# Kernel tuning notes

Measured on AMD Instinct MI355X. Metric: run time of the kernel, lower is better.

## Reference

```python
import jax, jax.numpy as jnp
import numpy as np

N, E, F_IN = 100000, 600000, 128
HID, NCLS = 128, 2
# ratio=0.8 applied three times: ceil(0.8*100000), ceil(0.8*80000), ceil(0.8*64000)
K1, K2, K3 = 80000, 64000, 51200


def setup_inputs() -> dict:
    key = jax.random.key(0)
    k = jax.random.split(key, 16)
    s = 0.05
    p = {}
    p['x'] = jax.random.normal(k[0], (N, F_IN), dtype=jnp.float32)
    p['edge_index'] = jax.random.randint(k[1], (2, E), 0, N)
    # GraphConv i: out = lin_rel(sum_j x_j) + lin_root(x_i); lin_root has no bias (PyG)
    p['Wr1'] = jax.random.normal(k[2], (HID, F_IN), jnp.float32) * s
    p['br1'] = jnp.zeros((HID,), jnp.float32)
    p['Wroot1'] = jax.random.normal(k[3], (HID, F_IN), jnp.float32) * s
    p['pw1'] = jax.random.normal(k[4], (HID,), jnp.float32) * s
    p['Wr2'] = jax.random.normal(k[5], (HID, HID), jnp.float32) * s
    p['br2'] = jnp.zeros((HID,), jnp.float32)
    p['Wroot2'] = jax.random.normal(k[6], (HID, HID), jnp.float32) * s
    p['pw2'] = jax.random.normal(k[7], (HID,), jnp.float32) * s
    p['Wr3'] = jax.random.normal(k[8], (HID, HID), jnp.float32) * s
    p['br3'] = jnp.zeros((HID,), jnp.float32)
    p['Wroot3'] = jax.random.normal(k[9], (HID, HID), jnp.float32) * s
    p['pw3'] = jax.random.normal(k[10], (HID,), jnp.float32) * s
    p['W_lin1'] = jax.random.normal(k[11], (HID, 2 * HID), jnp.float32) * s
    p['b_lin1'] = jnp.zeros((HID,), jnp.float32)
    p['W_lin2'] = jax.random.normal(k[12], (64, HID), jnp.float32) * s
    p['b_lin2'] = jnp.zeros((64,), jnp.float32)
    p['W_lin3'] = jax.random.normal(k[13], (NCLS, 64), jnp.float32) * s
    p['b_lin3'] = jnp.zeros((NCLS,), jnp.float32)
    return p


def _gconv(x, src, dst, emask, Wr, br, Wroot):
    # PyG GraphConv(aggr='add'): masked edges contribute zero (== removed edge)
    msg = x[src] * emask[:, None].astype(x.dtype)           # [E, F]
    agg = jax.ops.segment_sum(msg, dst, num_segments=x.shape[0])
    return agg @ Wr.T + br + x @ Wroot.T


def _topk_pool(x, src, dst, emask, w, k):
    # PyG TopKPooling: score = tanh((x.w)/||w||); keep top-k nodes; x = x[perm]*score[perm]
    score = jnp.tanh((x @ w) / jnp.linalg.norm(w))
    vals, perm = jax.lax.top_k(score, k)
    x_new = x[perm] * vals[:, None]
    new_idx = jnp.full((x.shape[0],), -1, jnp.int32).at[perm].set(
        jnp.arange(k, dtype=jnp.int32))
    ns, nd = new_idx[src], new_idx[dst]
    valid = emask & (ns >= 0) & (nd >= 0)
    return x_new, jnp.where(valid, ns, 0), jnp.where(valid, nd, 0), valid


def _readout(x):
    # single graph (batch=None): gmp || gap -> [1, 2F]
    return jnp.concatenate([x.max(axis=0), x.mean(axis=0)])[None, :]


def reference(x, edge_index, Wr1, br1, Wroot1, pw1, Wr2, br2, Wroot2, pw2,
              Wr3, br3, Wroot3, pw3, W_lin1, b_lin1, W_lin2, b_lin2, W_lin3, b_lin3):
    src = edge_index[0].astype(jnp.int32)
    dst = edge_index[1].astype(jnp.int32)
    emask = jnp.ones((src.shape[0],), dtype=bool)

    h = jax.nn.relu(_gconv(x, src, dst, emask, Wr1, br1, Wroot1))
    h, src, dst, emask = _topk_pool(h, src, dst, emask, pw1, K1)
    r1 = _readout(h)

    h = jax.nn.relu(_gconv(h, src, dst, emask, Wr2, br2, Wroot2))
    h, src, dst, emask = _topk_pool(h, src, dst, emask, pw2, K2)
    r2 = _readout(h)

    h = jax.nn.relu(_gconv(h, src, dst, emask, Wr3, br3, Wroot3))
    h, src, dst, emask = _topk_pool(h, src, dst, emask, pw3, K3)
    r3 = _readout(h)

    z = r1 + r2 + r3                                        # [1, 256]
    z = jax.nn.relu(z @ W_lin1.T + b_lin1)                  # dropout: inference no-op
    z = jax.nn.relu(z @ W_lin2.T + b_lin2)
    return z @ W_lin3.T + b_lin3                            # [1, num_classes]
```

## Files before the change

kernel.cpp:

```cpp
#include <hip/hip_runtime.h>
#include <hip/hip_bf16.h>
#include <math.h>

#define N0 100000
#define E0 600000
#define KP1 80000
#define KP2 64000
#define KP3 51200
#define F 128
#define SCAN_CHUNK 1024
#define NCHUNK ((N0 + SCAN_CHUNK - 1) / SCAN_CHUNK)
#define MAXGB 6400

typedef __attribute__((ext_vector_type(8))) short short8;
typedef __attribute__((ext_vector_type(8))) unsigned short ushort8;
typedef __attribute__((ext_vector_type(4))) float f32x4;

__device__ __forceinline__ unsigned fkey(float f) {
    unsigned u = __float_as_uint(f);
    return u ^ ((u & 0x80000000u) ? 0xFFFFFFFFu : 0x80000000u);
}
__device__ __forceinline__ unsigned short f2b(float f) {
    __hip_bfloat16 h = __float2bfloat16(f);
    return *(unsigned short*)&h;
}
__device__ __forceinline__ float b2f(unsigned short u) {
    __hip_bfloat16 h;
    *(unsigned short*)&h = u;
    return __bfloat162float(h);
}

__global__ __launch_bounds__(256) void cvt4K(const float* __restrict__ in,
                                             unsigned short* __restrict__ out, int n4,
                                             unsigned* __restrict__ bar, unsigned* __restrict__ hist,
                                             unsigned* __restrict__ cnt, int* __restrict__ orig) {
    int i = blockIdx.x * 256 + threadIdx.x;
    if (blockIdx.x == 0) {
        if (threadIdx.x < 16) bar[threadIdx.x] = 0u;
        hist[threadIdx.x] = 0u;
    }
    if (i < N0) { cnt[i] = 0u; orig[i] = i; }
    if (i >= n4) return;
    float4 v = *(const float4*)(in + (size_t)i * 4);
    *(ushort4*)(out + (size_t)i * 4) = make_ushort4(f2b(v.x), f2b(v.y), f2b(v.z), f2b(v.w));
}

__global__ __launch_bounds__(256) void cvtWAllK(const float* __restrict__ a0, const float* __restrict__ a1,
                                                const float* __restrict__ a2, const float* __restrict__ a3,
                                                const float* __restrict__ a4, const float* __restrict__ a5,
                                                unsigned short* __restrict__ o) {
    int m = blockIdx.y;
    const float* src = (m == 0) ? a0 : (m == 1) ? a1 : (m == 2) ? a2 : (m == 3) ? a3 : (m == 4) ? a4 : a5;
    int i = blockIdx.x * 256 + threadIdx.x;
    float4 v = *(const float4*)(src + (size_t)i * 4);
    *(ushort4*)(o + (size_t)m * 16384 + (size_t)i * 4) = make_ushort4(f2b(v.x), f2b(v.y), f2b(v.z), f2b(v.w));
}

__global__ __launch_bounds__(128) void pwnK(const float* __restrict__ p0, const float* __restrict__ p1,
                                            const float* __restrict__ p2, float* __restrict__ pwn) {
    __shared__ float sh[128];
    int l = blockIdx.x, t = threadIdx.x;
    const float* p = (l == 0) ? p0 : (l == 1) ? p1 : p2;
    float v = p[t];
    sh[t] = v * v;
    __syncthreads();
    for (int off = 64; off; off >>= 1) {
        if (t < off) sh[t] += sh[t + off];
        __syncthreads();
    }
    pwn[l * 128 + t] = v / sqrtf(sh[0]);
}

__global__ __launch_bounds__(256) void histDstK(const int* __restrict__ dst, unsigned* __restrict__ cnt) {
    int e = blockIdx.x * 256 + threadIdx.x;
    if (e < E0) atomicAdd(&cnt[dst[e]], 1u);
}

__global__ __launch_bounds__(256) void scanReduceK(const unsigned* __restrict__ cnt,
                                                   unsigned* __restrict__ chunkSum, int nbins) {
    __shared__ unsigned sh[256];
    int base = blockIdx.x * SCAN_CHUNK + threadIdx.x * 4;
    unsigned s = 0;
#pragma unroll
    for (int i = 0; i < 4; i++) { int b = base + i; if (b < nbins) s += cnt[b]; }
    sh[threadIdx.x] = s;
    __syncthreads();
    for (int off = 128; off; off >>= 1) {
        if (threadIdx.x < off) sh[threadIdx.x] += sh[threadIdx.x + off];
        __syncthreads();
    }
    if (threadIdx.x == 0) chunkSum[blockIdx.x] = sh[0];
}

__global__ void scanChunksK(const unsigned* __restrict__ chunkSum, unsigned* __restrict__ chunkOff,
                            int nchunks, unsigned* __restrict__ totalOut) {
    if (threadIdx.x == 0) {
        unsigned run = 0;
        for (int i = 0; i < nchunks; i++) { chunkOff[i] = run; run += chunkSum[i]; }
        *totalOut = run;
    }
}

__global__ __launch_bounds__(256) void scanFinalK(const unsigned* __restrict__ cntIn,
                                                  unsigned* __restrict__ cnt,
                                                  const unsigned* __restrict__ chunkOff,
                                                  unsigned* __restrict__ rowptr, int nbins) {
    __shared__ unsigned sh[256];
    int t = threadIdx.x;
    int base = blockIdx.x * SCAN_CHUNK + t * 4;
    unsigned c[4], s = 0;
#pragma unroll
    for (int i = 0; i < 4; i++) { int b = base + i; c[i] = (b < nbins) ? cntIn[b] : 0u; s += c[i]; }
    sh[t] = s;
    __syncthreads();
    for (int off = 1; off < 256; off <<= 1) {
        unsigned v = (t >= off) ? sh[t - off] : 0u;
        __syncthreads();
        sh[t] += v;
        __syncthreads();
    }
    unsigned basep = chunkOff[blockIdx.x] + sh[t] - s;
#pragma unroll
    for (int i = 0; i < 4; i++) {
        int b = base + i;
        if (b < nbins) { rowptr[b] = basep; basep += c[i]; cnt[b] = 0u; }
    }
}

__global__ __launch_bounds__(256) void scatterFillK(const int* __restrict__ src,
                                                    const int* __restrict__ dst,
                                                    const unsigned* __restrict__ rowptr,
                                                    unsigned* __restrict__ fill,
                                                    int* __restrict__ sortedSrc) {
    int e = blockIdx.x * 256 + threadIdx.x;
    if (e >= E0) return;
    int d = dst[e];
    unsigned p = rowptr[d] + atomicAdd(&fill[d], 1u);
    sortedSrc[p] = src[e];
}

__global__ __launch_bounds__(256) void aggSegB(const unsigned short* __restrict__ x,
                                               const int* __restrict__ srcCur,
                                               const unsigned* __restrict__ rowptr,
                                               const int* __restrict__ orig,
                                               unsigned short* __restrict__ agg, int n) {
    int g = blockIdx.x * 16 + (threadIdx.x >> 4);
    int q = threadIdx.x & 15;
    if (g >= n) return;
    int d = orig[g];
    unsigned e0 = rowptr[d], e1 = rowptr[d + 1];
    float a[8];
#pragma unroll
    for (int j = 0; j < 8; j++) a[j] = 0.f;
    unsigned e = e0;
    for (; e + 4 <= e1; e += 4) {
        int s0 = srcCur[e], s1 = srcCur[e + 1], s2 = srcCur[e + 2], s3 = srcCur[e + 3];
        ushort8 v0 = *(const ushort8*)(x + (size_t)(s0 < 0 ? 0 : s0) * F + q * 8);
        ushort8 v1 = *(const ushort8*)(x + (size_t)(s1 < 0 ? 0 : s1) * F + q * 8);
        ushort8 v2 = *(const ushort8*)(x + (size_t)(s2 < 0 ? 0 : s2) * F + q * 8);
        ushort8 v3 = *(const ushort8*)(x + (size_t)(s3 < 0 ? 0 : s3) * F + q * 8);
        float m0 = s0 < 0 ? 0.f : 1.f, m1 = s1 < 0 ? 0.f : 1.f;
        float m2 = s2 < 0 ? 0.f : 1.f, m3 = s3 < 0 ? 0.f : 1.f;
#pragma unroll
        for (int j = 0; j < 8; j++) {
            a[j] = fmaf(b2f(v0[j]), m0, a[j]);
            a[j] = fmaf(b2f(v1[j]), m1, a[j]);
            a[j] = fmaf(b2f(v2[j]), m2, a[j]);
            a[j] = fmaf(b2f(v3[j]), m3, a[j]);
        }
    }
    for (; e < e1; e++) {
        int s = srcCur[e];
        if (s < 0) continue;
        ushort8 v = *(const ushort8*)(x + (size_t)s * F + q * 8);
#pragma unroll
        for (int j = 0; j < 8; j++) a[j] += b2f(v[j]);
    }
    ushort8 o;
#pragma unroll
    for (int j = 0; j < 8; j++) o[j] = f2b(a[j]);
    *(ushort8*)(agg + (size_t)g * F + q * 8) = o;
}

#define CPAD 40
__global__ __launch_bounds__(256) void convM(const unsigned short* __restrict__ A0,
                                             const unsigned short* __restrict__ A1,
                                             const unsigned short* __restrict__ W0,
                                             const unsigned short* __restrict__ W1,
                                             const float* __restrict__ br,
                                             const float* __restrict__ pwn,
                                             unsigned short* __restrict__ hbf,
                                             float* __restrict__ sc,
                                             unsigned* __restrict__ keys,
                                             unsigned* __restrict__ hist,
                                             unsigned* __restrict__ st,
                                             unsigned* __restrict__ done,
                                             int n, int k, int nbGrid) {
    __shared__ unsigned short As[128 * CPAD];
    __shared__ unsigned short Bs[128 * CPAD];
    __shared__ unsigned selh[256];
    int tid = threadIdx.x;
    int w = tid >> 6, l = tid & 63;
    int r = l & 15, g = l >> 4;
    int bm = blockIdx.x * 128;
    int srow = tid >> 2, q4 = tid & 3;

    selh[tid] = 0u;

    f32x4 acc[2][8];
#pragma unroll
    for (int m = 0; m < 2; m++)
#pragma unroll
        for (int c = 0; c < 8; c++) acc[m][c] = (f32x4){0.f, 0.f, 0.f, 0.f};

    for (int ph = 0; ph < 2; ph++) {
        const unsigned short* A = ph ? A1 : A0;
        const unsigned short* W = ph ? W1 : W0;
        for (int kk = 0; kk < 128; kk += 32) {
            __syncthreads();
#pragma unroll
            for (int h2 = 0; h2 < 2; h2++) {
                int rr = srow + h2 * 64;
                uint4 av = make_uint4(0u, 0u, 0u, 0u);
                if (bm + rr < n) av = *(const uint4*)(A + (size_t)(bm + rr) * F + kk + q4 * 8);
                *(uint4*)(&As[rr * CPAD + q4 * 8]) = av;
                uint4 wv = *(const uint4*)(W + (size_t)rr * F + kk + q4 * 8);
                *(uint4*)(&Bs[rr * CPAD + q4 * 8]) = wv;
            }
            __syncthreads();
            short8 af[2], bf[8];
#pragma unroll
            for (int m = 0; m < 2; m++)
                af[m] = *(const short8*)(&As[(w * 32 + m * 16 + r) * CPAD + g * 8]);
#pragma unroll
            for (int c = 0; c < 8; c++)
                bf[c] = *(const short8*)(&Bs[(c * 16 + r) * CPAD + g * 8]);
#pragma unroll
            for (int m = 0; m < 2; m++)
#pragma unroll
                for (int c = 0; c < 8; c++)
                    acc[m][c] = __builtin_amdgcn_mfma_f32_16x16x32_bf16(af[m], bf[c], acc[m][c], 0, 0, 0);
        }
    }

    float pd[2][4];
#pragma unroll
    for (int m = 0; m < 2; m++)
#pragma unroll
        for (int j = 0; j < 4; j++) pd[m][j] = 0.f;

#pragma unroll
    for (int c = 0; c < 8; c++) {
        int col = c * 16 + r;
        float bias = br[col];
        float pwc = pwn[col];
#pragma unroll
        for (int m = 0; m < 2; m++) {
#pragma unroll
            for (int j = 0; j < 4; j++) {
                int row = bm + w * 32 + m * 16 + g * 4 + j;
                float h = fmaxf(acc[m][c][j] + bias, 0.f);
                pd[m][j] += h * pwc;
                if (row < n) hbf[(size_t)row * F + col] = f2b(h);
            }
        }
    }
#pragma unroll
    for (int m = 0; m < 2; m++) {
#pragma unroll
        for (int j = 0; j < 4; j++) {
            float p = pd[m][j];
            p += __shfl_xor(p, 1);
            p += __shfl_xor(p, 2);
            p += __shfl_xor(p, 4);
            p += __shfl_xor(p, 8);
            if (r == 0) {
                int row = bm + w * 32 + m * 16 + g * 4 + j;
                if (row < n) {
                    float s = tanhf(p);
                    sc[row] = s;
                    unsigned key = fkey(s);
                    keys[row] = key;
                    atomicAdd(&selh[key >> 24], 1u);
                }
            }
        }
    }

    __syncthreads();
    if (selh[tid]) atomicAdd(&hist[tid], selh[tid]);
    __syncthreads();
    __shared__ bool lastS;
    if (tid == 0) {
        __threadfence();
        lastS = (atomicAdd(done, 1u) == (unsigned)(nbGrid - 1));
    }
    __syncthreads();
    if (!lastS) return;
    selh[tid] = atomicExch(&hist[tid], 0u);
    __syncthreads();
    if (tid == 0) {
        unsigned krem = (unsigned)k, cum = 0, pfx = 0;
        for (int bch = 255; bch >= 0; bch--) {
            unsigned cc = selh[bch];
            if (cum + cc >= krem) {
                pfx = ((unsigned)bch) << 24;
                krem -= cum;
                break;
            }
            cum += cc;
        }
        atomicExch(&st[0], pfx);
        atomicExch(&st[1], krem);
        *done = 0u;
    }
}

__global__ __launch_bounds__(256) void histSelK(const unsigned* __restrict__ keys, int n,
                                                int p, unsigned* __restrict__ st,
                                                unsigned* __restrict__ hist,
                                                unsigned* __restrict__ done, int nb) {
    __shared__ unsigned lh[256];
    __shared__ bool last;
    int tid = threadIdx.x;
    lh[tid] = 0;
    __syncthreads();
    unsigned prefix = st[0];
    int i = blockIdx.x * 256 + tid;
    if (i < n) {
        unsigned key = keys[i];
        bool m = ((key >> (32 - 8 * p)) == (prefix >> (32 - 8 * p)));
        if (m) atomicAdd(&lh[(key >> (24 - 8 * p)) & 255u], 1u);
    }
    __syncthreads();
    if (lh[tid]) atomicAdd(&hist[tid], lh[tid]);
    __syncthreads();
    if (tid == 0) {
        __threadfence();
        last = (atomicAdd(done, 1u) == (unsigned)(nb - 1));
    }
    __syncthreads();
    if (!last) return;
    lh[tid] = atomicExch(&hist[tid], 0u);
    __syncthreads();
    if (tid == 0) {
        unsigned krem = st[1], cum = 0;
        for (int b = 255; b >= 0; b--) {
            unsigned c = lh[b];
            if (cum + c >= krem) {
                st[0] |= ((unsigned)b) << (24 - 8 * p);
                st[1] = krem - cum;
                break;
            }
            cum += c;
        }
        *done = 0u;
    }
}

__global__ __launch_bounds__(256) void countsK(const unsigned* __restrict__ keys, int n,
                                               const unsigned* __restrict__ st,
                                               unsigned* __restrict__ bGT, unsigned* __restrict__ bEQ,
                                               unsigned* __restrict__ sGT, unsigned* __restrict__ sEQ,
                                               unsigned* __restrict__ done, int nb) {
    __shared__ int cg_, ce_;
    __shared__ bool last;
    int tid = threadIdx.x;
    if (tid == 0) { cg_ = 0; ce_ = 0; }
    __syncthreads();
    unsigned t = st[0];
    int g = 0, e = 0;
    for (int it = 0; it < 4; it++) {
        int i = blockIdx.x * 1024 + it * 256 + tid;
        if (i < n) {
            unsigned k = keys[i];
            g += (k > t);
            e += (k == t);
        }
    }
    atomicAdd(&cg_, g);
    atomicAdd(&ce_, e);
    __syncthreads();
    if (tid == 0) {
        bGT[blockIdx.x] = (unsigned)cg_;
        bEQ[blockIdx.x] = (unsigned)ce_;
        __threadfence();
        last = (atomicAdd(done, 1u) == (unsigned)(nb - 1));
    }
    __syncthreads();
    if (!last) return;
    if (tid == 0) {
        unsigned gs = 0, es = 0;
        for (int b = 0; b < nb; b++) {
            atomicExch(&sGT[b], gs);
            atomicExch(&sEQ[b], es);
            gs += atomicAdd(&bGT[b], 0u);
            es += atomicAdd(&bEQ[b], 0u);
        }
        *done = 0u;
    }
}

__global__ __launch_bounds__(256) void markOrigK(const unsigned* __restrict__ keys, int n,
                                                 const unsigned* __restrict__ st,
                                                 const unsigned* __restrict__ sGT,
                                                 const unsigned* __restrict__ sEQ,
                                                 int* __restrict__ nidx,
                                                 const int* __restrict__ origIn,
                                                 int* __restrict__ origOut, int doNext) {
    __shared__ int wG[4], wE[4];
    __shared__ int runG, runE;
    int tid = threadIdx.x, wv = tid >> 6, lane = tid & 63;
    if (tid == 0) { runG = 0; runE = 0; }
    unsigned t = st[0];
    int needEq = (int)st[1];
    int gOff = (int)atomicAdd((unsigned*)&sGT[blockIdx.x], 0u);
    int eOff = (int)atomicAdd((unsigned*)&sEQ[blockIdx.x], 0u);
    unsigned long long mlt = (((unsigned long long)1) << lane) - 1ull;
    __syncthreads();
    for (int it = 0; it < 4; it++) {
        int i = blockIdx.x * 1024 + it * 256 + tid;
        bool inb = i < n;
        unsigned k = inb ? keys[i] : 0u;
        bool pG = inb && (k > t), pE = inb && (k == t);
        unsigned long long bG = __ballot(pG), bE = __ballot(pE);
        int lpG = __popcll(bG & mlt), lpE = __popcll(bE & mlt);
        if (lane == 0) { wG[wv] = __popcll(bG); wE[wv] = __popcll(bE); }
        __syncthreads();
        int woG = 0, woE = 0;
        for (int w = 0; w < wv; w++) { woG += wG[w]; woE += wE[w]; }
        int gB = gOff + runG + woG + lpG;
        int eB = eOff + runE + woE + lpE;
        int ni = -1;
        if (pG) ni = gB + (eB < needEq ? eB : needEq);
        else if (pE && eB < needEq) ni = gB + eB;
        if (inb) {
            nidx[i] = ni;
            if (doNext && ni >= 0) origOut[ni] = origIn[i];
        }
        __syncthreads();
        if (tid == 0) {
            runG += wG[0] + wG[1] + wG[2] + wG[3];
            runE += wE[0] + wE[1] + wE[2] + wE[3];
        }
        __syncthreads();
    }
}

__global__ __launch_bounds__(256) void gatherRK(const unsigned short* __restrict__ hbf,
                                                const float* __restrict__ sc,
                                                const int* __restrict__ nidx,
                                                const int* __restrict__ srcIn,
                                                int* __restrict__ srcOut,
                                                unsigned short* __restrict__ bufB,
                                                float* __restrict__ pmax, float* __restrict__ psum,
                                                int n, int doNext) {
    __shared__ float redm[256 * 8];
    __shared__ float reds[256 * 8];
    int tid = threadIdx.x, b = blockIdx.x;
    int q = tid & 15;
    int i = b * 16 + (tid >> 4);
    float lm[8], ls[8];
#pragma unroll
    for (int j = 0; j < 8; j++) { lm[j] = -INFINITY; ls[j] = 0.f; }
    if (i < n) {
        int ni = nidx[i];
        if (ni >= 0) {
            float s = sc[i];
            ushort8 v = *(const ushort8*)(hbf + (size_t)i * F + q * 8);
            ushort8 o;
#pragma unroll
            for (int j = 0; j < 8; j++) {
                float prod = b2f(v[j]) * s;
                o[j] = f2b(prod);
                lm[j] = fmaxf(lm[j], prod);
                ls[j] += prod;
            }
            *(ushort8*)(bufB + (size_t)ni * F + q * 8) = o;
        }
    }
    if (doNext) {
        int nbg = gridDim.x;
        for (int e = b * 256 + tid; e < E0; e += nbg * 256) {
            int s2 = srcIn[e];
            srcOut[e] = (s2 >= 0) ? nidx[s2] : -1;
        }
    }
#pragma unroll
    for (int j = 0; j < 8; j++) { redm[tid * 8 + j] = lm[j]; reds[tid * 8 + j] = ls[j]; }
    __syncthreads();
    if (tid < 16) {
        for (int g2 = 1; g2 < 16; g2++) {
#pragma unroll
            for (int j = 0; j < 8; j++) {
                lm[j] = fmaxf(lm[j], redm[(g2 * 16 + tid) * 8 + j]);
                ls[j] += reds[(g2 * 16 + tid) * 8 + j];
            }
        }
#pragma unroll
        for (int j = 0; j < 8; j++) {
            pmax[(size_t)b * 128 + tid * 8 + j] = lm[j];
            psum[(size_t)b * 128 + tid * 8 + j] = ls[j];
        }
    }
}

__global__ __launch_bounds__(128) void rfinal2K(const float* __restrict__ pmax,
                                                const float* __restrict__ psum,
                                                unsigned* __restrict__ pm2, unsigned* __restrict__ ps2,
                                                float* __restrict__ r, unsigned* __restrict__ done,
                                                int np, int k, int initR) {
    int t = threadIdx.x, b = blockIdx.x;
    float m = -INFINITY, s = 0.f;
    for (int row = b; row < np; row += 64) {
        m = fmaxf(m, pmax[(size_t)row * 128 + t]);
        s += psum[(size_t)row * 128 + t];
    }
    atomicExch(&pm2[b * 128 + t], __float_as_uint(m));
    atomicExch(&ps2[b * 128 + t], __float_as_uint(s));
    __syncthreads();
    __shared__ bool last;
    if (t == 0) {
        __threadfence();
        last = (atomicAdd(done, 1u) == 63u);
    }
    __syncthreads();
    if (!last) return;
    m = -INFINITY; s = 0.f;
    for (int bb = 0; bb < 64; bb++) {
        m = fmaxf(m, __uint_as_float(atomicAdd(&pm2[bb * 128 + t], 0u)));
        s += __uint_as_float(atomicAdd(&ps2[bb * 128 + t], 0u));
    }
    if (initR) { r[t] = m; r[128 + t] = s / (float)k; }
    else       { r[t] += m; r[128 + t] += s / (float)k; }
    if (t == 0) *done = 0u;
}

__global__ __launch_bounds__(256) void mlpK(const float* __restrict__ r,
                                            const float* __restrict__ W1, const float* __restrict__ b1,
                                            const float* __restrict__ W2, const float* __restrict__ b2,
                                            const float* __restrict__ W3, const float* __restrict__ b3,
                                            float* __restrict__ out) {
    __shared__ float z0[256], z1[128], z2[64];
    int t = threadIdx.x;
    z0[t] = r[t];
    __syncthreads();
    if (t < 128) {
        float a = b1[t];
        for (int kk = 0; kk < 256; kk++) a = fmaf(W1[t * 256 + kk], z0[kk], a);
        z1[t] = fmaxf(a, 0.f);
    }
    __syncthreads();
    if (t < 64) {
        float a = b2[t];
        for (int kk = 0; kk < 128; kk++) a = fmaf(W2[t * 128 + kk], z1[kk], a);
        z2[t] = fmaxf(a, 0.f);
    }
    __syncthreads();
    if (t < 2) {
        float a = b3[t];
        for (int kk = 0; kk < 64; kk++) a = fmaf(W3[t * 64 + kk], z2[kk], a);
        out[t] = a;
    }
}

extern "C" void kernel_launch(void* const* d_in, const int* in_sizes, int n_in,
                              void* d_out, int out_size, void* d_ws, size_t ws_size,
                              hipStream_t stream) {
    const float* x = (const float*)d_in[0];
    const int* ei = (const int*)d_in[1];
    const float* Wr[3]    = { (const float*)d_in[2],  (const float*)d_in[6],  (const float*)d_in[10] };
    const float* br[3]    = { (const float*)d_in[3],  (const float*)d_in[7],  (const float*)d_in[11] };
    const float* Wroot[3] = { (const float*)d_in[4],  (const float*)d_in[8],  (const float*)d_in[12] };
    const float* pw[3]    = { (const float*)d_in[5],  (const float*)d_in[9],  (const float*)d_in[13] };
    const float* W1 = (const float*)d_in[14];
    const float* b1 = (const float*)d_in[15];
    const float* W2 = (const float*)d_in[16];
    const float* b2 = (const float*)d_in[17];
    const float* W3 = (const float*)d_in[18];
    const float* b3 = (const float*)d_in[19];
    float* out = (float*)d_out;
    char* w = (char*)d_ws;

    size_t o = 0;
    auto alc = [&](size_t bytes) { size_t r = o; o += (bytes + 255) & ~(size_t)255; return r; };
    unsigned short* hbf    = (unsigned short*)(w + alc((size_t)N0 * F * 2));
    unsigned short* xbf    = (unsigned short*)(w + alc((size_t)N0 * F * 2));
    unsigned short* aggbf  = (unsigned short*)(w + alc((size_t)N0 * F * 2));
    unsigned short* bufBbf = (unsigned short*)(w + alc((size_t)KP1 * F * 2));
    unsigned short* wbf    = (unsigned short*)(w + alc((size_t)6 * 16384 * 2));
    float*    pwn    = (float*)(w + alc(3 * 128 * 4));
    float*    sc     = (float*)(w + alc((size_t)N0 * 4));
    unsigned* keys   = (unsigned*)(w + alc((size_t)N0 * 4));
    int*      nidx   = (int*)(w + alc((size_t)N0 * 4));
    int*      sSrc0  = (int*)(w + alc((size_t)E0 * 4));
    int*      srcCA  = (int*)(w + alc((size_t)E0 * 4));
    int*      srcCB  = (int*)(w + alc((size_t)E0 * 4));
    unsigned* cnt    = (unsigned*)(w + alc((size_t)N0 * 4));
    unsigned* rowptr = (unsigned*)(w + alc((size_t)(N0 + 1) * 4));
    int*      origA  = (int*)(w + alc((size_t)N0 * 4));
    int*      origB  = (int*)(w + alc((size_t)N0 * 4));
    unsigned* chS    = (unsigned*)(w + alc(NCHUNK * 4));
    unsigned* chO    = (unsigned*)(w + alc(NCHUNK * 4));
    unsigned* hist   = (unsigned*)(w + alc(256 * 4));
    unsigned* st     = (unsigned*)(w + alc(64));
    unsigned* barA   = (unsigned*)(w + alc(16 * 4));
    unsigned* bGT    = (unsigned*)(w + alc(128 * 4));
    unsigned* bEQ    = (unsigned*)(w + alc(128 * 4));
    unsigned* sGT    = (unsigned*)(w + alc(128 * 4));
    unsigned* sEQ    = (unsigned*)(w + alc(128 * 4));
    float*    r      = (float*)(w + alc(256 * 4));
    float*    pmax   = (float*)(w + alc((size_t)MAXGB * F * 4));
    float*    psum   = (float*)(w + alc((size_t)MAXGB * F * 4));
    unsigned* pm2    = (unsigned*)(w + alc(64 * 128 * 4));
    unsigned* ps2    = (unsigned*)(w + alc(64 * 128 * 4));
    if (o > ws_size) return;

    const int* srcOrig = ei;
    const int* dstOrig = ei + E0;

    cvt4K<<<(N0 * F / 4 + 255) / 256, 256, 0, stream>>>(x, xbf, N0 * F / 4, barA, hist, cnt, origA);
    cvtWAllK<<<dim3(16, 6), 256, 0, stream>>>(Wr[0], Wroot[0], Wr[1], Wroot[1], Wr[2], Wroot[2], wbf);
    pwnK<<<3, 128, 0, stream>>>(pw[0], pw[1], pw[2], pwn);
    histDstK<<<(E0 + 255) / 256, 256, 0, stream>>>(dstOrig, cnt);
    scanReduceK<<<NCHUNK, 256, 0, stream>>>(cnt, chS, N0);
    scanChunksK<<<1, 1, 0, stream>>>(chS, chO, NCHUNK, rowptr + N0);
    scanFinalK<<<NCHUNK, 256, 0, stream>>>(cnt, cnt, chO, rowptr, N0);
    scatterFillK<<<(E0 + 255) / 256, 256, 0, stream>>>(srcOrig, dstOrig, rowptr, cnt, sSrc0);

    unsigned* doneA = barA + 8;

    const int ns[3] = { N0, KP1, KP2 };
    const int ks[3] = { KP1, KP2, KP3 };
    const int* srcCur[3] = { sSrc0, srcCA, srcCB };
    int* srcNext[3] = { srcCA, srcCB, srcCA };
    const int* origCur[3] = { origA, origB, origA };
    int* origNext[3] = { origB, origA, origB };

    for (int L = 0; L < 3; L++) {
        int n = ns[L], k = ks[L];
        const unsigned short* xinbf = (L == 0) ? xbf : bufBbf;
        int doNext = (L < 2) ? 1 : 0;

        aggSegB<<<(n + 15) / 16, 256, 0, stream>>>(xinbf, srcCur[L], rowptr, origCur[L], aggbf, n);
        int nbc = (n + 127) / 128;
        convM<<<nbc, 256, 0, stream>>>(aggbf, xinbf,
                                       wbf + (size_t)(L * 2) * 16384,
                                       wbf + (size_t)(L * 2 + 1) * 16384,
                                       br[L], pwn + L * 128, hbf, sc, keys,
                                       hist, st, doneA, n, k, nbc);
        int nbh = (n + 255) / 256;
        for (int p = 1; p < 4; p++)
            histSelK<<<nbh, 256, 0, stream>>>(keys, n, p, st, hist, doneA, nbh);
        int nb = (n + 1023) / 1024;
        countsK<<<nb, 256, 0, stream>>>(keys, n, st, bGT, bEQ, sGT, sEQ, doneA, nb);
        markOrigK<<<nb, 256, 0, stream>>>(keys, n, st, sGT, sEQ, nidx, origCur[L], origNext[L], doNext);
        int nbg = (n + 15) / 16;
        gatherRK<<<nbg, 256, 0, stream>>>(hbf, sc, nidx, srcCur[L], srcNext[L], bufBbf, pmax, psum, n, doNext);
        rfinal2K<<<64, 128, 0, stream>>>(pmax, psum, pm2, ps2, r, doneA, nbg, k, (L == 0) ? 1 : 0);
    }

    mlpK<<<1, 256, 0, stream>>>(r, W1, b1, W2, b2, W3, b3, out);
}
```

Measured before the change: 718.0 us.

## Preload full weight tile in LDS and coalesce convM output stores via LDS

```diff
diff --git a/kernel.cpp b/kernel.cpp
--- a/kernel.cpp
+++ b/kernel.cpp
@@ -183,6 +183,7 @@
 }
 
 #define CPAD 40
+#define BSTR 136
 __global__ __launch_bounds__(256) void convM(const unsigned short* __restrict__ A0,
                                              const unsigned short* __restrict__ A1,
                                              const unsigned short* __restrict__ W0,
@@ -196,8 +197,10 @@
                                              unsigned* __restrict__ st,
                                              unsigned* __restrict__ done,
                                              int n, int k, int nbGrid) {
-    __shared__ unsigned short As[128 * CPAD];
-    __shared__ unsigned short Bs[128 * CPAD];
+    __shared__ union {
+        struct { unsigned short As[128 * CPAD]; unsigned short Bs[128 * BSTR]; } s;
+        unsigned short Cs[128 * BSTR];
+    } u;
     __shared__ unsigned selh[256];
     int tid = threadIdx.x;
     int w = tid >> 6, l = tid & 63;
@@ -216,25 +219,32 @@
     for (int ph = 0; ph < 2; ph++) {
         const unsigned short* A = ph ? A1 : A0;
         const unsigned short* W = ph ? W1 : W0;
+        __syncthreads();
+        {
+            int col = tid >> 1, hf = tid & 1;
+#pragma unroll
+            for (int i2 = 0; i2 < 8; i2++) {
+                uint4 wv = *(const uint4*)(W + (size_t)col * F + hf * 64 + i2 * 8);
+                *(uint4*)(&u.s.Bs[col * BSTR + hf * 64 + i2 * 8]) = wv;
+            }
+        }
         for (int kk = 0; kk < 128; kk += 32) {
-            __syncthreads();
+            if (kk) __syncthreads();
 #pragma unroll
             for (int h2 = 0; h2 < 2; h2++) {
                 int rr = srow + h2 * 64;
                 uint4 av = make_uint4(0u, 0u, 0u, 0u);
                 if (bm + rr < n) av = *(const uint4*)(A + (size_t)(bm + rr) * F + kk + q4 * 8);
-                *(uint4*)(&As[rr * CPAD + q4 * 8]) = av;
-                uint4 wv = *(const uint4*)(W + (size_t)rr * F + kk + q4 * 8);
-                *(uint4*)(&Bs[rr * CPAD + q4 * 8]) = wv;
+                *(uint4*)(&u.s.As[rr * CPAD + q4 * 8]) = av;
             }
             __syncthreads();
             short8 af[2], bf[8];
 #pragma unroll
             for (int m = 0; m < 2; m++)
-                af[m] = *(const short8*)(&As[(w * 32 + m * 16 + r) * CPAD + g * 8]);
+                af[m] = *(const short8*)(&u.s.As[(w * 32 + m * 16 + r) * CPAD + g * 8]);
 #pragma unroll
             for (int c = 0; c < 8; c++)
-                bf[c] = *(const short8*)(&Bs[(c * 16 + r) * CPAD + g * 8]);
+                bf[c] = *(const short8*)(&u.s.Bs[(c * 16 + r) * BSTR + kk + g * 8]);
 #pragma unroll
             for (int m = 0; m < 2; m++)
 #pragma unroll
@@ -249,6 +259,7 @@
 #pragma unroll
         for (int j = 0; j < 4; j++) pd[m][j] = 0.f;
 
+    __syncthreads();
 #pragma unroll
     for (int c = 0; c < 8; c++) {
         int col = c * 16 + r;
@@ -258,10 +269,22 @@
         for (int m = 0; m < 2; m++) {
 #pragma unroll
             for (int j = 0; j < 4; j++) {
-                int row = bm + w * 32 + m * 16 + g * 4 + j;
+                int rl = w * 32 + m * 16 + g * 4 + j;
                 float h = fmaxf(acc[m][c][j] + bias, 0.f);
                 pd[m][j] += h * pwc;
-                if (row < n) hbf[(size_t)row * F + col] = f2b(h);
+                u.Cs[rl * BSTR + col] = f2b(h);
+            }
+        }
+    }
+    __syncthreads();
+    {
+        int rl = tid >> 1, hf = tid & 1;
+        int grow = bm + rl;
+        if (grow < n) {
+#pragma unroll
+            for (int i2 = 0; i2 < 8; i2++) {
+                uint4 v = *(const uint4*)(&u.Cs[rl * BSTR + hf * 64 + i2 * 8]);
+                *(uint4*)(&hbf[(size_t)grow * F + hf * 64 + i2 * 8]) = v;
             }
         }
     }
@@ -365,6 +388,7 @@
                                                unsigned* __restrict__ done, int nb) {
     __shared__ int cg_, ce_;
     __shared__ bool last;
+    __shared__ unsigned sgl[128], seq[128];
     int tid = threadIdx.x;
     if (tid == 0) { cg_ = 0; ce_ = 0; }
     __syncthreads();
@@ -389,13 +413,15 @@
     }
     __syncthreads();
     if (!last) return;
+    if (tid < nb && tid < 128) { sgl[tid] = atomicAdd(&bGT[tid], 0u); seq[tid] = atomicAdd(&bEQ[tid], 0u); }
+    __syncthreads();
     if (tid == 0) {
         unsigned gs = 0, es = 0;
         for (int b = 0; b < nb; b++) {
             atomicExch(&sGT[b], gs);
             atomicExch(&sEQ[b], es);
-            gs += atomicAdd(&bGT[b], 0u);
-            es += atomicAdd(&bEQ[b], 0u);
+            gs += sgl[b];
+            es += seq[b];
         }
         *done = 0u;
     }
@@ -527,6 +553,7 @@
     __syncthreads();
     if (!last) return;
     m = -INFINITY; s = 0.f;
+#pragma unroll 8
     for (int bb = 0; bb < 64; bb++) {
         m = fmaxf(m, __uint_as_float(atomicAdd(&pm2[bb * 128 + t], 0u)));
         s += __uint_as_float(atomicAdd(&ps2[bb * 128 + t], 0u));
```

Result: faster. 642.0 us (-10.6%).

## Shrink conv GEMM tile to 64 rows, prefetch K-slices, swap MFMA operands

Applied to the files above, without the earlier changes.

```diff
diff --git a/kernel.cpp b/kernel.cpp
--- a/kernel.cpp
+++ b/kernel.cpp
@@ -196,95 +196,76 @@
                                              unsigned* __restrict__ st,
                                              unsigned* __restrict__ done,
                                              int n, int k, int nbGrid) {
-    __shared__ unsigned short As[128 * CPAD];
+    __shared__ unsigned short As[64 * CPAD];
     __shared__ unsigned short Bs[128 * CPAD];
     __shared__ unsigned selh[256];
     int tid = threadIdx.x;
     int w = tid >> 6, l = tid & 63;
     int r = l & 15, g = l >> 4;
-    int bm = blockIdx.x * 128;
+    int bm = blockIdx.x * 64;
     int srow = tid >> 2, q4 = tid & 3;
 
     selh[tid] = 0u;
 
-    f32x4 acc[2][8];
-#pragma unroll
-    for (int m = 0; m < 2; m++)
-#pragma unroll
-        for (int c = 0; c < 8; c++) acc[m][c] = (f32x4){0.f, 0.f, 0.f, 0.f};
-
+    f32x4 acc[8];
+#pragma unroll
+    for (int c = 0; c < 8; c++) acc[c] = (f32x4){0.f, 0.f, 0.f, 0.f};
+
+    int rowA = bm + srow;
     for (int ph = 0; ph < 2; ph++) {
         const unsigned short* A = ph ? A1 : A0;
         const unsigned short* W = ph ? W1 : W0;
-        for (int kk = 0; kk < 128; kk += 32) {
+        uint4 av = make_uint4(0u, 0u, 0u, 0u);
+        if (rowA < n) av = *(const uint4*)(A + (size_t)rowA * F + q4 * 8);
+        uint4 wv0 = *(const uint4*)(W + (size_t)srow * F + q4 * 8);
+        uint4 wv1 = *(const uint4*)(W + (size_t)(srow + 64) * F + q4 * 8);
+        for (int kki = 0; kki < 4; kki++) {
             __syncthreads();
-#pragma unroll
-            for (int h2 = 0; h2 < 2; h2++) {
-                int rr = srow + h2 * 64;
-                uint4 av = make_uint4(0u, 0u, 0u, 0u);
-                if (bm + rr < n) av = *(const uint4*)(A + (size_t)(bm + rr) * F + kk + q4 * 8);
-                *(uint4*)(&As[rr * CPAD + q4 * 8]) = av;
-                uint4 wv = *(const uint4*)(W + (size_t)rr * F + kk + q4 * 8);
-                *(uint4*)(&Bs[rr * CPAD + q4 * 8]) = wv;
+            *(uint4*)(&As[srow * CPAD + q4 * 8]) = av;
+            *(uint4*)(&Bs[srow * CPAD + q4 * 8]) = wv0;
+            *(uint4*)(&Bs[(srow + 64) * CPAD + q4 * 8]) = wv1;
+            if (kki < 3) {
+                int kn = (kki + 1) * 32;
+                av = make_uint4(0u, 0u, 0u, 0u);
+                if (rowA < n) av = *(const uint4*)(A + (size_t)rowA * F + kn + q4 * 8);
+                wv0 = *(const uint4*)(W + (size_t)srow * F + kn + q4 * 8);
+                wv1 = *(const uint4*)(W + (size_t)(srow + 64) * F + kn + q4 * 8);
             }
             __syncthreads();
-            short8 af[2], bf[8];
-#pragma unroll
-            for (int m = 0; m < 2; m++)
-                af[m] = *(const short8*)(&As[(w * 32 + m * 16 + r) * CPAD + g * 8]);
+            short8 af = *(const short8*)(&As[(w * 16 + r) * CPAD + g * 8]);
+            short8 bf[8];
 #pragma unroll
             for (int c = 0; c < 8; c++)
                 bf[c] = *(const short8*)(&Bs[(c * 16 + r) * CPAD + g * 8]);
 #pragma unroll
-            for (int m = 0; m < 2; m++)
-#pragma unroll
-                for (int c = 0; c < 8; c++)
-                    acc[m][c] = __builtin_amdgcn_mfma_f32_16x16x32_bf16(af[m], bf[c], acc[m][c], 0, 0, 0);
-        }
-    }
-
-    float pd[2][4];
-#pragma unroll
-    for (int m = 0; m < 2; m++)
-#pragma unroll
-        for (int j = 0; j < 4; j++) pd[m][j] = 0.f;
-
+            for (int c = 0; c < 8; c++)
+                acc[c] = __builtin_amdgcn_mfma_f32_16x16x32_bf16(bf[c], af, acc[c], 0, 0, 0);
+        }
+    }
+
+    int row = bm + w * 16 + r;
+    bool rowOK = row < n;
+    float pd = 0.f;
 #pragma unroll
     for (int c = 0; c < 8; c++) {
-        int col = c * 16 + r;
-        float bias = br[col];
-        float pwc = pwn[col];
-#pragma unroll
-        for (int m = 0; m < 2; m++) {
-#pragma unroll
-            for (int j = 0; j < 4; j++) {
-                int row = bm + w * 32 + m * 16 + g * 4 + j;
-                float h = fmaxf(acc[m][c][j] + bias, 0.f);
-                pd[m][j] += h * pwc;
-                if (row < n) hbf[(size_t)row * F + col] = f2b(h);
-            }
-        }
-    }
-#pragma unroll
-    for (int m = 0; m < 2; m++) {
-#pragma unroll
-        for (int j = 0; j < 4; j++) {
-            float p = pd[m][j];
-            p += __shfl_xor(p, 1);
-            p += __shfl_xor(p, 2);
-            p += __shfl_xor(p, 4);
-            p += __shfl_xor(p, 8);
-            if (r == 0) {
-                int row = bm + w * 32 + m * 16 + g * 4 + j;
-                if (row < n) {
-                    float s = tanhf(p);
-                    sc[row] = s;
-                    unsigned key = fkey(s);
-                    keys[row] = key;
-                    atomicAdd(&selh[key >> 24], 1u);
-                }
-            }
-        }
+        int colb = c * 16 + g * 4;
+        float h0 = fmaxf(acc[c][0] + br[colb + 0], 0.f);
+        float h1 = fmaxf(acc[c][1] + br[colb + 1], 0.f);
+        float h2 = fmaxf(acc[c][2] + br[colb + 2], 0.f);
+        float h3 = fmaxf(acc[c][3] + br[colb + 3], 0.f);
+        pd += h0 * pwn[colb + 0] + h1 * pwn[colb + 1] + h2 * pwn[colb + 2] + h3 * pwn[colb + 3];
+        if (rowOK)
+            *(ushort4*)(&hbf[(size_t)row * F + colb]) =
+                make_ushort4(f2b(h0), f2b(h1), f2b(h2), f2b(h3));
+    }
+    pd += __shfl_xor(pd, 16);
+    pd += __shfl_xor(pd, 32);
+    if (l < 16 && rowOK) {
+        float s = tanhf(pd);
+        sc[row] = s;
+        unsigned key = fkey(s);
+        keys[row] = key;
+        atomicAdd(&selh[key >> 24], 1u);
     }
 
     __syncthreads();
@@ -365,6 +346,7 @@
                                                unsigned* __restrict__ done, int nb) {
     __shared__ int cg_, ce_;
     __shared__ bool last;
+    __shared__ unsigned sgl[128], seq[128];
     int tid = threadIdx.x;
     if (tid == 0) { cg_ = 0; ce_ = 0; }
     __syncthreads();
@@ -389,13 +371,15 @@
     }
     __syncthreads();
     if (!last) return;
+    if (tid < nb && tid < 128) { sgl[tid] = atomicAdd(&bGT[tid], 0u); seq[tid] = atomicAdd(&bEQ[tid], 0u); }
+    __syncthreads();
     if (tid == 0) {
         unsigned gs = 0, es = 0;
         for (int b = 0; b < nb; b++) {
             atomicExch(&sGT[b], gs);
             atomicExch(&sEQ[b], es);
-            gs += atomicAdd(&bGT[b], 0u);
-            es += atomicAdd(&bEQ[b], 0u);
+            gs += sgl[b];
+            es += seq[b];
         }
         *done = 0u;
     }
@@ -527,6 +511,7 @@
     __syncthreads();
     if (!last) return;
     m = -INFINITY; s = 0.f;
+#pragma unroll 8
     for (int bb = 0; bb < 64; bb++) {
         m = fmaxf(m, __uint_as_float(atomicAdd(&pm2[bb * 128 + t], 0u)));
         s += __uint_as_float(atomicAdd(&ps2[bb * 128 + t], 0u));
@@ -643,7 +628,7 @@
         int doNext = (L < 2) ? 1 : 0;
 
         aggSegB<<<(n + 15) / 16, 256, 0, stream>>>(xinbf, srcCur[L], rowptr, origCur[L], aggbf, n);
-        int nbc = (n + 127) / 128;
+        int nbc = (n + 63) / 64;
         convM<<<nbc, 256, 0, stream>>>(aggbf, xinbf,
                                        wbf + (size_t)(L * 2) * 16384,
                                        wbf + (size_t)(L * 2 + 1) * 16384,
```

Result: faster. 683.4 us (-4.8%).
